# Performance work log

Hardware: AMD Instinct MI355X
Metric: run time of the kernel (lower is better)

Reference implementation:

```python
import jax, jax.numpy as jnp
import numpy as np

BN_EPS = 1e-5


def _gin_layer(x, agg, W1, b1, W2, b2, gamma, beta):
    # GINConv with eps=0: h = MLP(x + sum_{j in N(i)} x_j)
    h = x + agg
    h = jax.nn.relu(h @ W1 + b1)
    h = jax.nn.relu(h @ W2 + b2)
    # BatchNorm1d, training mode (batch statistics, biased variance)
    mean = jnp.mean(h, axis=0)
    var = jnp.var(h, axis=0)
    return (h - mean) * jax.lax.rsqrt(var + BN_EPS) * gamma + beta


def setup_inputs() -> dict:
    key = jax.random.key(0)
    ks = jax.random.split(key, 10)
    N, E, D_IN, D_H, D_OUT = 100000, 1600000, 128, 128, 128
    s = lambda fi, fo: (2.0 / (fi + fo)) ** 0.5
    return {
        "x": jax.random.normal(ks[0], (N, D_IN), dtype=jnp.float32),
        "edge_index": jax.random.randint(ks[1], (2, E), 0, N, dtype=jnp.int64),
        "W1a": jax.random.normal(ks[2], (D_IN, D_H), dtype=jnp.float32) * s(D_IN, D_H),
        "b1a": jnp.zeros((D_H,), jnp.float32),
        "W1b": jax.random.normal(ks[3], (D_H, D_H), dtype=jnp.float32) * s(D_H, D_H),
        "b1b": jnp.zeros((D_H,), jnp.float32),
        "g1": jnp.ones((D_H,), jnp.float32),
        "be1": jnp.zeros((D_H,), jnp.float32),
        "W2a": jax.random.normal(ks[4], (D_H, D_H), dtype=jnp.float32) * s(D_H, D_H),
        "b2a": jnp.zeros((D_H,), jnp.float32),
        "W2b": jax.random.normal(ks[5], (D_H, D_OUT), dtype=jnp.float32) * s(D_H, D_OUT),
        "b2b": jnp.zeros((D_OUT,), jnp.float32),
        "g2": jnp.ones((D_OUT,), jnp.float32),
        "be2": jnp.zeros((D_OUT,), jnp.float32),
    }


def reference(x, edge_index, W1a, b1a, W1b, b1b, g1, be1,
              W2a, b2a, W2b, b2b, g2, be2):
    N = x.shape[0]
    src, dst = edge_index[0], edge_index[1]
    # layer 1: scatter-add neighbor features into targets
    agg = jax.ops.segment_sum(x[src], dst, num_segments=N)
    h = _gin_layer(x, agg, W1a, b1a, W1b, b1b, g1, be1)
    # layer 2
    agg = jax.ops.segment_sum(h[src], dst, num_segments=N)
    h = _gin_layer(h, agg, W2a, b2a, W2b, b2b, g2, be2)
    return h
```

## Files before the change

kernel.cpp:

```cpp
#include <hip/hip_runtime.h>
#include <hip/hip_bf16.h>

typedef unsigned int u32;
typedef unsigned short u16;
typedef short bf16x8 __attribute__((ext_vector_type(8)));
typedef float f32x4 __attribute__((ext_vector_type(4)));

static __device__ __forceinline__ float bf_lo(u32 v) { return __uint_as_float(v << 16); }
static __device__ __forceinline__ float bf_hi(u32 v) { return __uint_as_float(v & 0xffff0000u); }
static __device__ __forceinline__ u16 f2bf(float f) {
    u32 u = __float_as_uint(f);
    u32 r = u + 0x7fffu + ((u >> 16) & 1u);
    return (u16)(r >> 16);
}
static __device__ __forceinline__ u32 pack2(float a, float b) {
    return ((u32)f2bf(b) << 16) | (u32)f2bf(a);
}

__global__ __launch_bounds__(256) void prep_k(const float* __restrict__ x,
                                              u32* __restrict__ out2, int total4,
                                              const int* __restrict__ edst,
                                              int* __restrict__ gcount, int E, int NB,
                                              const float* __restrict__ Wa,
                                              const float* __restrict__ Wb,
                                              const float* __restrict__ Wc,
                                              const float* __restrict__ Wd,
                                              u16* __restrict__ Wf)
{
    int b = blockIdx.x, t = threadIdx.x;
    if (b < 2048) {
        for (int i = b * 256 + t; i < total4; i += 2048 * 256) {
            float4 v = reinterpret_cast<const float4*>(x)[i];
            out2[2 * i + 0] = pack2(v.x, v.y);
            out2[2 * i + 1] = pack2(v.z, v.w);
        }
    } else if (b < 2304) {
        __shared__ int lh[1024];
        for (int i = t; i < 1024; i += 256) lh[i] = 0;
        __syncthreads();
        for (int e = (b - 2048) * 256 + t; e < E; e += 256 * 256)
            atomicAdd(&lh[edst[e] >> 7], 1);
        __syncthreads();
        for (int bb = t; bb < NB; bb += 256)
            if (lh[bb]) atomicAdd(&gcount[bb], lh[bb]);
    } else {
        int g = (b - 2304) * 256 + t;
        int which = g >> 14;
        int tt = g & 16383;
        const float* W = which == 0 ? Wa : which == 1 ? Wb : which == 2 ? Wc : Wd;
        int j  = tt & 7;
        int l  = (tt >> 3) & 63;
        int nb = (tt >> 9) & 7;
        int kg = (tt >> 12) & 3;
        int k  = kg * 32 + (l >> 4) * 8 + j;
        int n  = nb * 16 + (l & 15);
        Wf[g] = f2bf(W[k * 128 + n]);
    }
}

__global__ __launch_bounds__(1024) void bscan_k(const int* __restrict__ gcount,
                                                int* __restrict__ goffs,
                                                int* __restrict__ gcur, int NB)
{
    __shared__ int s[1024];
    int t = threadIdx.x;
    int v = (t < NB) ? gcount[t] : 0;
    s[t] = v; __syncthreads();
    for (int d = 1; d < 1024; d <<= 1) {
        int x = (t >= d) ? s[t - d] : 0;
        __syncthreads();
        s[t] += x;
        __syncthreads();
    }
    if (t < NB) { int o = s[t] - v; goffs[t] = o; gcur[t] = o; }
    if (t == NB - 1) goffs[NB] = s[t];
}

__global__ __launch_bounds__(256) void bfill_k(const int* __restrict__ esrc,
                                               const int* __restrict__ edst,
                                               int* __restrict__ gcur,
                                               u32* __restrict__ bpacked, int E, int NB)
{
    __shared__ int lh[1024];
    __shared__ int lbase[1024];
    int t = threadIdx.x;
    for (int i = t; i < 1024; i += 256) lh[i] = 0;
    __syncthreads();
    int per = (E + gridDim.x - 1) / gridDim.x;
    int lo = blockIdx.x * per;
    int hi = lo + per; if (hi > E) hi = E;
    for (int e = lo + t; e < hi; e += 256) atomicAdd(&lh[edst[e] >> 7], 1);
    __syncthreads();
    for (int b = t; b < NB; b += 256) {
        int c = lh[b];
        lbase[b] = c ? atomicAdd(&gcur[b], c) : 0;
    }
    __syncthreads();
    for (int i = t; i < 1024; i += 256) lh[i] = 0;
    __syncthreads();
    for (int e = lo + t; e < hi; e += 256) {
        int d = edst[e];
        int b = d >> 7;
        int idx = atomicAdd(&lh[b], 1);
        bpacked[lbase[b] + idx] = ((u32)(d & 127) << 17) | (u32)esrc[e];
    }
}

__global__ __launch_bounds__(256) void fsort_k(const u32* __restrict__ bpacked,
                                               const int* __restrict__ goffs,
                                               int* __restrict__ slots,
                                               int* __restrict__ offs,
                                               int* __restrict__ deg, int N)
{
    __shared__ int cnt[128];
    __shared__ int roff[128];
    __shared__ int sb[128];
    int b = blockIdx.x, t = threadIdx.x;
    int start = goffs[b], end = goffs[b + 1];
    if (t < 128) cnt[t] = 0;
    __syncthreads();
    for (int e = start + t; e < end; e += 256)
        atomicAdd(&cnt[bpacked[e] >> 17], 1);
    __syncthreads();
    if (t < 128) sb[t] = cnt[t];
    __syncthreads();
    for (int d = 1; d < 128; d <<= 1) {
        int x = (t < 128 && t >= d) ? sb[t - d] : 0;
        __syncthreads();
        if (t < 128) sb[t] += x;
        __syncthreads();
    }
    if (t < 128) roff[t] = sb[t] - cnt[t];
    __syncthreads();
    int row0 = b * 128;
    if (t < 128 && row0 + t < N) {
        offs[row0 + t] = start + roff[t];
        deg[row0 + t]  = cnt[t];
    }
    if (t < 128) cnt[t] = 0;
    __syncthreads();
    for (int e = start + t; e < end; e += 256) {
        u32 pk = bpacked[e];
        int local = (int)(pk >> 17);
        int idx = atomicAdd(&cnt[local], 1);
        slots[start + roff[local] + idx] = (int)(pk & 0x1FFFF);
    }
}

#define ROWP(s) reinterpret_cast<const u32*>(xbase + ((size_t)(u32)(s) << 8))

template<int MODE>
__global__ __launch_bounds__(256) void gather_k(const u32* __restrict__ xb2,
                                                const int* __restrict__ offs,
                                                const int* __restrict__ deg,
                                                const int* __restrict__ slots,
                                                const float* __restrict__ stats_in,
                                                const float* __restrict__ g_in,
                                                const float* __restrict__ be_in,
                                                u32* __restrict__ xa2, int N)
{
    __shared__ float sc[128], sh[128];
    int t = threadIdx.x;
    if (MODE == 1) {
        if (t < 128) {
            float invN = 1.0f / (float)N;
            float mean = stats_in[t] * invN;
            float var  = stats_in[128 + t] * invN - mean * mean;
            float s = g_in[t] * rsqrtf(var + 1e-5f);
            sc[t] = s;
            sh[t] = be_in[t] - mean * s;
        }
        __syncthreads();
    }

    int row = blockIdx.x * 4 + (t >> 6);
    if (row >= N) return;
    int lane = t & 63;
    const char* xbase = (const char*)xb2;

    u32 self = ROWP(row)[lane];
    float ax0 = bf_lo(self), ay0 = bf_hi(self);
    float ax1 = 0.f, ay1 = 0.f, ax2 = 0.f, ay2 = 0.f, ax3 = 0.f, ay3 = 0.f;

    int ustart = __builtin_amdgcn_readfirstlane(offs[row]);
    int udg    = __builtin_amdgcn_readfirstlane(deg[row]);

    int e = 0;
    for (; e + 16 <= udg; e += 16) {
        int s0 = slots[ustart + e + 0],  s1 = slots[ustart + e + 1];
        int s2 = slots[ustart + e + 2],  s3 = slots[ustart + e + 3];
        int s4 = slots[ustart + e + 4],  s5 = slots[ustart + e + 5];
        int s6 = slots[ustart + e + 6],  s7 = slots[ustart + e + 7];
        int s8 = slots[ustart + e + 8],  s9 = slots[ustart + e + 9];
        int sA = slots[ustart + e + 10], sB = slots[ustart + e + 11];
        int sC = slots[ustart + e + 12], sD = slots[ustart + e + 13];
        int sE = slots[ustart + e + 14], sF = slots[ustart + e + 15];
        u32 v0 = ROWP(s0)[lane], v1 = ROWP(s1)[lane];
        u32 v2 = ROWP(s2)[lane], v3 = ROWP(s3)[lane];
        u32 v4 = ROWP(s4)[lane], v5 = ROWP(s5)[lane];
        u32 v6 = ROWP(s6)[lane], v7 = ROWP(s7)[lane];
        u32 v8 = ROWP(s8)[lane], v9 = ROWP(s9)[lane];
        u32 vA = ROWP(sA)[lane], vB = ROWP(sB)[lane];
        u32 vC = ROWP(sC)[lane], vD = ROWP(sD)[lane];
        u32 vE = ROWP(sE)[lane], vF = ROWP(sF)[lane];
        ax0 += bf_lo(v0); ay0 += bf_hi(v0);  ax1 += bf_lo(v1); ay1 += bf_hi(v1);
        ax2 += bf_lo(v2); ay2 += bf_hi(v2);  ax3 += bf_lo(v3); ay3 += bf_hi(v3);
        ax0 += bf_lo(v4); ay0 += bf_hi(v4);  ax1 += bf_lo(v5); ay1 += bf_hi(v5);
        ax2 += bf_lo(v6); ay2 += bf_hi(v6);  ax3 += bf_lo(v7); ay3 += bf_hi(v7);
        ax0 += bf_lo(v8); ay0 += bf_hi(v8);  ax1 += bf_lo(v9); ay1 += bf_hi(v9);
        ax2 += bf_lo(vA); ay2 += bf_hi(vA);  ax3 += bf_lo(vB); ay3 += bf_hi(vB);
        ax0 += bf_lo(vC); ay0 += bf_hi(vC);  ax1 += bf_lo(vD); ay1 += bf_hi(vD);
        ax2 += bf_lo(vE); ay2 += bf_hi(vE);  ax3 += bf_lo(vF); ay3 += bf_hi(vF);
    }
    int k = udg - e;
    if (k) {
        int s0 = slots[ustart + e + 0],  s1 = slots[ustart + e + 1];
        int s2 = slots[ustart + e + 2],  s3 = slots[ustart + e + 3];
        int s4 = slots[ustart + e + 4],  s5 = slots[ustart + e + 5];
        int s6 = slots[ustart + e + 6],  s7 = slots[ustart + e + 7];
        int s8 = slots[ustart + e + 8],  s9 = slots[ustart + e + 9];
        int sA = slots[ustart + e + 10], sB = slots[ustart + e + 11];
        int sC = slots[ustart + e + 12], sD = slots[ustart + e + 13];
        int sE = slots[ustart + e + 14];
        u32 v0 = 0, v1 = 0, v2 = 0, v3 = 0, v4 = 0, v5 = 0, v6 = 0, v7 = 0;
        u32 v8 = 0, v9 = 0, vA = 0, vB = 0, vC = 0, vD = 0, vE = 0;
        v0 = ROWP(s0)[lane];
        if (k > 1)  v1 = ROWP(s1)[lane];
        if (k > 2)  v2 = ROWP(s2)[lane];
        if (k > 3)  v3 = ROWP(s3)[lane];
        if (k > 4)  v4 = ROWP(s4)[lane];
        if (k > 5)  v5 = ROWP(s5)[lane];
        if (k > 6)  v6 = ROWP(s6)[lane];
        if (k > 7)  v7 = ROWP(s7)[lane];
        if (k > 8)  v8 = ROWP(s8)[lane];
        if (k > 9)  v9 = ROWP(s9)[lane];
        if (k > 10) vA = ROWP(sA)[lane];
        if (k > 11) vB = ROWP(sB)[lane];
        if (k > 12) vC = ROWP(sC)[lane];
        if (k > 13) vD = ROWP(sD)[lane];
        if (k > 14) vE = ROWP(sE)[lane];
        ax0 += bf_lo(v0); ay0 += bf_hi(v0);  ax1 += bf_lo(v1); ay1 += bf_hi(v1);
        ax2 += bf_lo(v2); ay2 += bf_hi(v2);  ax3 += bf_lo(v3); ay3 += bf_hi(v3);
        ax0 += bf_lo(v4); ay0 += bf_hi(v4);  ax1 += bf_lo(v5); ay1 += bf_hi(v5);
        ax2 += bf_lo(v6); ay2 += bf_hi(v6);  ax3 += bf_lo(v7); ay3 += bf_hi(v7);
        ax0 += bf_lo(v8); ay0 += bf_hi(v8);  ax1 += bf_lo(v9); ay1 += bf_hi(v9);
        ax2 += bf_lo(vA); ay2 += bf_hi(vA);  ax3 += bf_lo(vB); ay3 += bf_hi(vB);
        ax0 += bf_lo(vC); ay0 += bf_hi(vC);  ax1 += bf_lo(vD); ay1 += bf_hi(vD);
        ax2 += bf_lo(vE); ay2 += bf_hi(vE);
    }

    float ax = (ax0 + ax1) + (ax2 + ax3);
    float ay = (ay0 + ay1) + (ay2 + ay3);
    if (MODE == 1) {
        float d1 = (float)(udg + 1);
        ax = sc[2 * lane]     * ax + d1 * sh[2 * lane];
        ay = sc[2 * lane + 1] * ay + d1 * sh[2 * lane + 1];
    }
    xa2[(size_t)row * 64 + lane] = pack2(ax, ay);
}

__global__ __launch_bounds__(256) void mlp_mfma_k(
    const u16* __restrict__ xa,
    const u16* __restrict__ wfa, const float* __restrict__ ba,
    const u16* __restrict__ wfb, const float* __restrict__ bb,
    u16* __restrict__ hb_out, float* __restrict__ partial, int N)
{
    __shared__ short ta[64 * 128];
    __shared__ float ssum[256];

    int t = threadIdx.x;
    int w = t >> 6, l = t & 63;
    int row0 = blockIdx.x * 64;

    for (int c = t; c < 1024; c += 256) {
        int r = c >> 4, ci = c & 15;
        int dst = (r * 128 + ci * 8) ^ ((r & 7) << 3);
        f32x4 v;
        if (row0 + r < N)
            v = *reinterpret_cast<const f32x4*>(xa + ((size_t)(row0 + r) * 128 + ci * 8));
        else
            v = f32x4{0.f, 0.f, 0.f, 0.f};
        *reinterpret_cast<f32x4*>(ta + dst) = v;
    }

    bf16x8 wf[2][4];
#pragma unroll
    for (int nr = 0; nr < 2; ++nr) {
        int nb = 2 * w + nr;
#pragma unroll
        for (int kg = 0; kg < 4; ++kg)
            wf[nr][kg] = *reinterpret_cast<const bf16x8*>(
                wfa + ((size_t)((kg * 8 + nb) * 64 + l)) * 8);
    }
    __syncthreads();

    int rr = l & 15;
    int kg8 = l >> 4;

    f32x4 acc[4][2];
#pragma unroll
    for (int mr = 0; mr < 4; ++mr)
#pragma unroll
        for (int nr = 0; nr < 2; ++nr)
            acc[mr][nr] = f32x4{0.f, 0.f, 0.f, 0.f};

#pragma unroll
    for (int mr = 0; mr < 4; ++mr) {
        int r = mr * 16 + rr;
        bf16x8 af[4];
#pragma unroll
        for (int kg = 0; kg < 4; ++kg) {
            int idx = (r * 128 + kg * 32 + kg8 * 8) ^ ((r & 7) << 3);
            af[kg] = *reinterpret_cast<const bf16x8*>(ta + idx);
        }
#pragma unroll
        for (int nr = 0; nr < 2; ++nr)
#pragma unroll
            for (int kg = 0; kg < 4; ++kg)
                acc[mr][nr] = __builtin_amdgcn_mfma_f32_16x16x32_bf16(
                    af[kg], wf[nr][kg], acc[mr][nr], 0, 0, 0);
    }
    __syncthreads();

    bf16x8 wf2[2][4];
#pragma unroll
    for (int nr = 0; nr < 2; ++nr) {
        int nb = 2 * w + nr;
#pragma unroll
        for (int kg = 0; kg < 4; ++kg)
            wf2[nr][kg] = *reinterpret_cast<const bf16x8*>(
                wfb + ((size_t)((kg * 8 + nb) * 64 + l)) * 8);
    }

    int colb = w * 32;
    float b0 = ba[colb + rr];
    float b1 = ba[colb + 16 + rr];
#pragma unroll
    for (int mr = 0; mr < 4; ++mr)
#pragma unroll
        for (int nr = 0; nr < 2; ++nr) {
            float bb_ = nr ? b1 : b0;
            int col = colb + nr * 16 + rr;
#pragma unroll
            for (int reg = 0; reg < 4; ++reg) {
                int row = mr * 16 + kg8 * 4 + reg;
                float v = fmaxf(acc[mr][nr][reg] + bb_, 0.0f);
                ta[(row * 128 + col) ^ ((row & 7) << 3)] = (short)f2bf(v);
            }
        }
    __syncthreads();

#pragma unroll
    for (int mr = 0; mr < 4; ++mr)
#pragma unroll
        for (int nr = 0; nr < 2; ++nr)
            acc[mr][nr] = f32x4{0.f, 0.f, 0.f, 0.f};

#pragma unroll
    for (int mr = 0; mr < 4; ++mr) {
        int r = mr * 16 + rr;
        bf16x8 af[4];
#pragma unroll
        for (int kg = 0; kg < 4; ++kg) {
            int idx = (r * 128 + kg * 32 + kg8 * 8) ^ ((r & 7) << 3);
            af[kg] = *reinterpret_cast<const bf16x8*>(ta + idx);
        }
#pragma unroll
        for (int nr = 0; nr < 2; ++nr)
#pragma unroll
            for (int kg = 0; kg < 4; ++kg)
                acc[mr][nr] = __builtin_amdgcn_mfma_f32_16x16x32_bf16(
                    af[kg], wf2[nr][kg], acc[mr][nr], 0, 0, 0);
    }

    float c0 = bb[colb + rr];
    float c1 = bb[colb + 16 + rr];
    float s0 = 0.f, q0 = 0.f, s1 = 0.f, q1 = 0.f;
#pragma unroll
    for (int mr = 0; mr < 4; ++mr) {
#pragma unroll
        for (int reg = 0; reg < 4; ++reg) {
            int row = row0 + mr * 16 + kg8 * 4 + reg;
            bool ok = row < N;
            float v0 = fmaxf(acc[mr][0][reg] + c0, 0.0f);
            float v1 = fmaxf(acc[mr][1][reg] + c1, 0.0f);
            if (ok) {
                hb_out[(size_t)row * 128 + colb + rr]      = f2bf(v0);
                hb_out[(size_t)row * 128 + colb + 16 + rr] = f2bf(v1);
                s0 += v0; q0 += v0 * v0;
                s1 += v1; q1 += v1 * v1;
            }
        }
    }
    s0 += __shfl_xor(s0, 16); s0 += __shfl_xor(s0, 32);
    q0 += __shfl_xor(q0, 16); q0 += __shfl_xor(q0, 32);
    s1 += __shfl_xor(s1, 16); s1 += __shfl_xor(s1, 32);
    q1 += __shfl_xor(q1, 16); q1 += __shfl_xor(q1, 32);
    if (kg8 == 0) {
        ssum[colb + rr]            = s0;
        ssum[128 + colb + rr]      = q0;
        ssum[colb + 16 + rr]       = s1;
        ssum[128 + colb + 16 + rr] = q1;
    }
    __syncthreads();
    partial[(size_t)blockIdx.x * 256 + t] = ssum[t];
}

__global__ __launch_bounds__(256) void reduce_k(const float* __restrict__ partial,
                                                float* __restrict__ stats, int nrows)
{
    int t = threadIdx.x;
    int chunk = (nrows + gridDim.x - 1) / gridDim.x;
    int lo = blockIdx.x * chunk;
    int hi = lo + chunk; if (hi > nrows) hi = nrows;
    float acc = 0.f;
    for (int r = lo; r < hi; ++r)
        acc += partial[(size_t)r * 256 + t];
    if (hi > lo) atomicAdd(&stats[t], acc);
}

__global__ __launch_bounds__(256) void bn_apply_bf_k(
    const u32* __restrict__ h2b, const float* __restrict__ stats,
    const float* __restrict__ gamma, const float* __restrict__ beta,
    float* __restrict__ out, int N)
{
    __shared__ float sc[128], sh[128];
    int t = threadIdx.x;
    if (t < 128) {
        float invN = 1.0f / (float)N;
        float mean = stats[t] * invN;
        float var  = stats[128 + t] * invN - mean * mean;
        float s = gamma[t] * rsqrtf(var + 1e-5f);
        sc[t] = s;
        sh[t] = beta[t] - mean * s;
    }
    __syncthreads();
    int total2 = N * 64;
    for (int i = blockIdx.x * 256 + t; i < total2; i += gridDim.x * 256) {
        u32 v = h2b[i];
        int c = (i & 63) * 2;
        float2 o;
        o.x = bf_lo(v) * sc[c]     + sh[c];
        o.y = bf_hi(v) * sc[c + 1] + sh[c + 1];
        reinterpret_cast<float2*>(out)[i] = o;
    }
}

extern "C" void kernel_launch(void* const* d_in, const int* in_sizes, int n_in,
                              void* d_out, int out_size, void* d_ws, size_t ws_size,
                              hipStream_t stream)
{
    const float* x   = (const float*)d_in[0];
    const int*   ei  = (const int*)d_in[1];
    const float* W1a = (const float*)d_in[2];
    const float* b1a = (const float*)d_in[3];
    const float* W1b = (const float*)d_in[4];
    const float* b1b = (const float*)d_in[5];
    const float* g1  = (const float*)d_in[6];
    const float* be1 = (const float*)d_in[7];
    const float* W2a = (const float*)d_in[8];
    const float* b2a = (const float*)d_in[9];
    const float* W2b = (const float*)d_in[10];
    const float* b2b = (const float*)d_in[11];
    const float* g2  = (const float*)d_in[12];
    const float* be2 = (const float*)d_in[13];

    const int N = in_sizes[0] / 128;
    const int E = in_sizes[1] / 2;
    const int* esrc = ei;
    const int* edst = ei + E;
    const int NB = (N + 127) >> 7;

    const int mblocks = (N + 63) / 64;
    const int gblocks = (N + 3) / 4;

    char* p = (char*)d_ws;
    const size_t featb = (size_t)N * 128 * sizeof(u16);
    u16* xa = (u16*)p;            p += featb;
    u16* h1 = (u16*)p;            p += featb;
    u16* xb = (u16*)p;            p += featb;
    u16* wf = (u16*)p;            p += 4 * 16384 * sizeof(u16);
    int* slots = (int*)p;         p += (size_t)E * sizeof(int) + 64;
    int* deg   = (int*)p;         p += (size_t)N * sizeof(int);
    int* offs  = (int*)p;         p += (size_t)N * sizeof(int);
    int* gcount = (int*)p;        p += 1024 * sizeof(int);
    int* goffs  = (int*)p;        p += 1032 * sizeof(int);
    int* gcur   = (int*)p;        p += 1024 * sizeof(int);
    float* stats = (float*)p;     p += 512 * sizeof(float);
    float* partial = (float*)p;   p += (size_t)mblocks * 256 * sizeof(float);
    u32* bpacked = (u32*)xa;

    u16* wf1a = wf;
    u16* wf1b = wf + 16384;
    u16* wf2a = wf + 32768;
    u16* wf2b = wf + 49152;
    float* stats1 = stats;
    float* stats2 = stats + 256;

    float* h = (float*)d_out;

    hipMemsetAsync(gcount, 0, 1024 * sizeof(int), stream);
    prep_k<<<2560, 256, 0, stream>>>(x, (u32*)xb, N * 32,
                                     edst, gcount, E, NB,
                                     W1a, W1b, W2a, W2b, wf);
    bscan_k<<<1, 1024, 0, stream>>>(gcount, goffs, gcur, NB);
    bfill_k<<<256, 256, 0, stream>>>(esrc, edst, gcur, bpacked, E, NB);
    fsort_k<<<NB, 256, 0, stream>>>(bpacked, goffs, slots, offs, deg, N);
    hipMemsetAsync(stats, 0, 512 * sizeof(float), stream);

    gather_k<0><<<gblocks, 256, 0, stream>>>((const u32*)xb, offs, deg, slots,
                                             nullptr, nullptr, nullptr, (u32*)xa, N);
    mlp_mfma_k<<<mblocks, 256, 0, stream>>>(xa, wf1a, b1a, wf1b, b1b,
                                            h1, partial, N);
    reduce_k<<<32, 256, 0, stream>>>(partial, stats1, mblocks);

    gather_k<1><<<gblocks, 256, 0, stream>>>((const u32*)h1, offs, deg, slots,
                                             stats1, g1, be1, (u32*)xa, N);
    mlp_mfma_k<<<mblocks, 256, 0, stream>>>(xa, wf2a, b2a, wf2b, b2b,
                                            h1, partial, N);
    reduce_k<<<32, 256, 0, stream>>>(partial, stats2, mblocks);

    bn_apply_bf_k<<<2048, 256, 0, stream>>>((const u32*)h1, stats2, g2, be2, h, N);
}
```

Measured before the change: 275.4 us.

## Pad CSR neighbor lists to multiples of 16 with zero-row sentinels

The CSR build now pads each row's neighbor list to a multiple of 16 entries, filling the extras with indices of zero rows appended after the feature buffers. This takes an extra count pass, a second scan and a split sort kernel. In exchange the gather loop has no predicated tail: it unrolls by 32 with one 16-wide remainder, aiming to remove divergent tail loads and give more loads in flight. The cost is extra slot memory, redundant zero-row loads (about 7.5 per row on average at degree 16), and two more kernel launches.

```diff
diff --git a/kernel.cpp b/kernel.cpp
--- a/kernel.cpp
+++ b/kernel.cpp
@@ -58,13 +58,13 @@
     }
 }
 
-__global__ __launch_bounds__(1024) void bscan_k(const int* __restrict__ gcount,
-                                                int* __restrict__ goffs,
-                                                int* __restrict__ gcur, int NB)
+__global__ __launch_bounds__(1024) void bscan_k(const int* __restrict__ cnt,
+                                                int* __restrict__ outoffs,
+                                                int* __restrict__ outcur, int n)
 {
     __shared__ int s[1024];
     int t = threadIdx.x;
-    int v = (t < NB) ? gcount[t] : 0;
+    int v = (t < n) ? cnt[t] : 0;
     s[t] = v; __syncthreads();
     for (int d = 1; d < 1024; d <<= 1) {
         int x = (t >= d) ? s[t - d] : 0;
@@ -72,8 +72,8 @@
         s[t] += x;
         __syncthreads();
     }
-    if (t < NB) { int o = s[t] - v; goffs[t] = o; gcur[t] = o; }
-    if (t == NB - 1) goffs[NB] = s[t];
+    if (t < n) { int o = s[t] - v; outoffs[t] = o; if (outcur) outcur[t] = o; }
+    if (t == n - 1) outoffs[n] = s[t];
 }
 
 __global__ __launch_bounds__(256) void bfill_k(const int* __restrict__ esrc,
@@ -106,23 +106,47 @@
     }
 }
 
-__global__ __launch_bounds__(256) void fsort_k(const u32* __restrict__ bpacked,
-                                               const int* __restrict__ goffs,
-                                               int* __restrict__ slots,
-                                               int* __restrict__ offs,
-                                               int* __restrict__ deg, int N)
+__global__ __launch_bounds__(256) void fsortA_k(const u32* __restrict__ bpacked,
+                                                const int* __restrict__ goffs,
+                                                int* __restrict__ deg,
+                                                int* __restrict__ pbtotal, int N)
+{
+    __shared__ int cnt[128];
+    __shared__ int red[256];
+    int b = blockIdx.x, t = threadIdx.x;
+    int start = goffs[b], end = goffs[b + 1];
+    if (t < 128) cnt[t] = 0;
+    __syncthreads();
+    for (int e = start + t; e < end; e += 256)
+        atomicAdd(&cnt[bpacked[e] >> 17], 1);
+    __syncthreads();
+    int row0 = b * 128;
+    if (t < 128 && row0 + t < N) deg[row0 + t] = cnt[t];
+    red[t] = (t < 128) ? ((cnt[t] + 15) & ~15) : 0;
+    __syncthreads();
+    for (int d = 128; d >= 1; d >>= 1) {
+        if (t < d) red[t] += red[t + d];
+        __syncthreads();
+    }
+    if (t == 0) pbtotal[b] = red[0];
+}
+
+__global__ __launch_bounds__(256) void fsortB_k(const u32* __restrict__ bpacked,
+                                                const int* __restrict__ goffs,
+                                                const int* __restrict__ pbase,
+                                                const int* __restrict__ deg,
+                                                int* __restrict__ slots,
+                                                int* __restrict__ offs, int N)
 {
     __shared__ int cnt[128];
     __shared__ int roff[128];
     __shared__ int sb[128];
     int b = blockIdx.x, t = threadIdx.x;
     int start = goffs[b], end = goffs[b + 1];
-    if (t < 128) cnt[t] = 0;
-    __syncthreads();
-    for (int e = start + t; e < end; e += 256)
-        atomicAdd(&cnt[bpacked[e] >> 17], 1);
-    __syncthreads();
-    if (t < 128) sb[t] = cnt[t];
+    int row0 = b * 128;
+    int myc = (t < 128 && row0 + t < N) ? deg[row0 + t] : 0;
+    int pd = (myc + 15) & ~15;
+    if (t < 128) { sb[t] = pd; cnt[t] = 0; }
     __syncthreads();
     for (int d = 1; d < 128; d <<= 1) {
         int x = (t < 128 && t >= d) ? sb[t - d] : 0;
@@ -130,20 +154,22 @@
         if (t < 128) sb[t] += x;
         __syncthreads();
     }
-    if (t < 128) roff[t] = sb[t] - cnt[t];
-    __syncthreads();
-    int row0 = b * 128;
-    if (t < 128 && row0 + t < N) {
-        offs[row0 + t] = start + roff[t];
-        deg[row0 + t]  = cnt[t];
-    }
-    if (t < 128) cnt[t] = 0;
+    int base = pbase[b];
+    if (t < 128) {
+        roff[t] = sb[t] - pd;
+        if (row0 + t < N) offs[row0 + t] = base + roff[t];
+    }
     __syncthreads();
     for (int e = start + t; e < end; e += 256) {
         u32 pk = bpacked[e];
         int local = (int)(pk >> 17);
         int idx = atomicAdd(&cnt[local], 1);
-        slots[start + roff[local] + idx] = (int)(pk & 0x1FFFF);
+        slots[base + roff[local] + idx] = (int)(pk & 0x1FFFF);
+    }
+    __syncthreads();
+    if (t < 128) {
+        int o = base + roff[t];
+        for (int i = myc; i < pd; ++i) slots[o + i] = N + (i & 15);
     }
 }
 
@@ -184,9 +210,60 @@
 
     int ustart = __builtin_amdgcn_readfirstlane(offs[row]);
     int udg    = __builtin_amdgcn_readfirstlane(deg[row]);
+    int pdg    = (udg + 15) & ~15;
 
     int e = 0;
-    for (; e + 16 <= udg; e += 16) {
+    for (; e + 32 <= pdg; e += 32) {
+        int s0 = slots[ustart + e + 0],  s1 = slots[ustart + e + 1];
+        int s2 = slots[ustart + e + 2],  s3 = slots[ustart + e + 3];
+        int s4 = slots[ustart + e + 4],  s5 = slots[ustart + e + 5];
+        int s6 = slots[ustart + e + 6],  s7 = slots[ustart + e + 7];
+        int s8 = slots[ustart + e + 8],  s9 = slots[ustart + e + 9];
+        int sA = slots[ustart + e + 10], sB = slots[ustart + e + 11];
+        int sC = slots[ustart + e + 12], sD = slots[ustart + e + 13];
+        int sE = slots[ustart + e + 14], sF = slots[ustart + e + 15];
+        int sG = slots[ustart + e + 16], sH = slots[ustart + e + 17];
+        int sI = slots[ustart + e + 18], sJ = slots[ustart + e + 19];
+        int sK = slots[ustart + e + 20], sL = slots[ustart + e + 21];
+        int sM = slots[ustart + e + 22], sN_ = slots[ustart + e + 23];
+        int sO = slots[ustart + e + 24], sP = slots[ustart + e + 25];
+        int sQ = slots[ustart + e + 26], sR = slots[ustart + e + 27];
+        int sS = slots[ustart + e + 28], sT = slots[ustart + e + 29];
+        int sU = slots[ustart + e + 30], sV = slots[ustart + e + 31];
+        u32 v0 = ROWP(s0)[lane], v1 = ROWP(s1)[lane];
+        u32 v2 = ROWP(s2)[lane], v3 = ROWP(s3)[lane];
+        u32 v4 = ROWP(s4)[lane], v5 = ROWP(s5)[lane];
+        u32 v6 = ROWP(s6)[lane], v7 = ROWP(s7)[lane];
+        u32 v8 = ROWP(s8)[lane], v9 = ROWP(s9)[lane];
+        u32 vA = ROWP(sA)[lane], vB = ROWP(sB)[lane];
+        u32 vC = ROWP(sC)[lane], vD = ROWP(sD)[lane];
+        u32 vE = ROWP(sE)[lane], vF = ROWP(sF)[lane];
+        u32 vG = ROWP(sG)[lane], vH = ROWP(sH)[lane];
+        u32 vI = ROWP(sI)[lane], vJ = ROWP(sJ)[lane];
+        u32 vK = ROWP(sK)[lane], vL = ROWP(sL)[lane];
+        u32 vM = ROWP(sM)[lane], vN = ROWP(sN_)[lane];
+        u32 vO = ROWP(sO)[lane], vP = ROWP(sP)[lane];
+        u32 vQ = ROWP(sQ)[lane], vR = ROWP(sR)[lane];
+        u32 vS = ROWP(sS)[lane], vT = ROWP(sT)[lane];
+        u32 vU = ROWP(sU)[lane], vV = ROWP(sV)[lane];
+        ax0 += bf_lo(v0); ay0 += bf_hi(v0);  ax1 += bf_lo(v1); ay1 += bf_hi(v1);
+        ax2 += bf_lo(v2); ay2 += bf_hi(v2);  ax3 += bf_lo(v3); ay3 += bf_hi(v3);
+        ax0 += bf_lo(v4); ay0 += bf_hi(v4);  ax1 += bf_lo(v5); ay1 += bf_hi(v5);
+        ax2 += bf_lo(v6); ay2 += bf_hi(v6);  ax3 += bf_lo(v7); ay3 += bf_hi(v7);
+        ax0 += bf_lo(v8); ay0 += bf_hi(v8);  ax1 += bf_lo(v9); ay1 += bf_hi(v9);
+        ax2 += bf_lo(vA); ay2 += bf_hi(vA);  ax3 += bf_lo(vB); ay3 += bf_hi(vB);
+        ax0 += bf_lo(vC); ay0 += bf_hi(vC);  ax1 += bf_lo(vD); ay1 += bf_hi(vD);
+        ax2 += bf_lo(vE); ay2 += bf_hi(vE);  ax3 += bf_lo(vF); ay3 += bf_hi(vF);
+        ax0 += bf_lo(vG); ay0 += bf_hi(vG);  ax1 += bf_lo(vH); ay1 += bf_hi(vH);
+        ax2 += bf_lo(vI); ay2 += bf_hi(vI);  ax3 += bf_lo(vJ); ay3 += bf_hi(vJ);
+        ax0 += bf_lo(vK); ay0 += bf_hi(vK);  ax1 += bf_lo(vL); ay1 += bf_hi(vL);
+        ax2 += bf_lo(vM); ay2 += bf_hi(vM);  ax3 += bf_lo(vN); ay3 += bf_hi(vN);
+        ax0 += bf_lo(vO); ay0 += bf_hi(vO);  ax1 += bf_lo(vP); ay1 += bf_hi(vP);
+        ax2 += bf_lo(vQ); ay2 += bf_hi(vQ);  ax3 += bf_lo(vR); ay3 += bf_hi(vR);
+        ax0 += bf_lo(vS); ay0 += bf_hi(vS);  ax1 += bf_lo(vT); ay1 += bf_hi(vT);
+        ax2 += bf_lo(vU); ay2 += bf_hi(vU);  ax3 += bf_lo(vV); ay3 += bf_hi(vV);
+    }
+    if (e < pdg) {
         int s0 = slots[ustart + e + 0],  s1 = slots[ustart + e + 1];
         int s2 = slots[ustart + e + 2],  s3 = slots[ustart + e + 3];
         int s4 = slots[ustart + e + 4],  s5 = slots[ustart + e + 5];
@@ -212,42 +289,6 @@
         ax0 += bf_lo(vC); ay0 += bf_hi(vC);  ax1 += bf_lo(vD); ay1 += bf_hi(vD);
         ax2 += bf_lo(vE); ay2 += bf_hi(vE);  ax3 += bf_lo(vF); ay3 += bf_hi(vF);
     }
-    int k = udg - e;
-    if (k) {
-        int s0 = slots[ustart + e + 0],  s1 = slots[ustart + e + 1];
-        int s2 = slots[ustart + e + 2],  s3 = slots[ustart + e + 3];
-        int s4 = slots[ustart + e + 4],  s5 = slots[ustart + e + 5];
-        int s6 = slots[ustart + e + 6],  s7 = slots[ustart + e + 7];
-        int s8 = slots[ustart + e + 8],  s9 = slots[ustart + e + 9];
-        int sA = slots[ustart + e + 10], sB = slots[ustart + e + 11];
-        int sC = slots[ustart + e + 12], sD = slots[ustart + e + 13];
-        int sE = slots[ustart + e + 14];
-        u32 v0 = 0, v1 = 0, v2 = 0, v3 = 0, v4 = 0, v5 = 0, v6 = 0, v7 = 0;
-        u32 v8 = 0, v9 = 0, vA = 0, vB = 0, vC = 0, vD = 0, vE = 0;
-        v0 = ROWP(s0)[lane];
-        if (k > 1)  v1 = ROWP(s1)[lane];
-        if (k > 2)  v2 = ROWP(s2)[lane];
-        if (k > 3)  v3 = ROWP(s3)[lane];
-        if (k > 4)  v4 = ROWP(s4)[lane];
-        if (k > 5)  v5 = ROWP(s5)[lane];
-        if (k > 6)  v6 = ROWP(s6)[lane];
-        if (k > 7)  v7 = ROWP(s7)[lane];
-        if (k > 8)  v8 = ROWP(s8)[lane];
-        if (k > 9)  v9 = ROWP(s9)[lane];
-        if (k > 10) vA = ROWP(sA)[lane];
-        if (k > 11) vB = ROWP(sB)[lane];
-        if (k > 12) vC = ROWP(sC)[lane];
-        if (k > 13) vD = ROWP(sD)[lane];
-        if (k > 14) vE = ROWP(sE)[lane];
-        ax0 += bf_lo(v0); ay0 += bf_hi(v0);  ax1 += bf_lo(v1); ay1 += bf_hi(v1);
-        ax2 += bf_lo(v2); ay2 += bf_hi(v2);  ax3 += bf_lo(v3); ay3 += bf_hi(v3);
-        ax0 += bf_lo(v4); ay0 += bf_hi(v4);  ax1 += bf_lo(v5); ay1 += bf_hi(v5);
-        ax2 += bf_lo(v6); ay2 += bf_hi(v6);  ax3 += bf_lo(v7); ay3 += bf_hi(v7);
-        ax0 += bf_lo(v8); ay0 += bf_hi(v8);  ax1 += bf_lo(v9); ay1 += bf_hi(v9);
-        ax2 += bf_lo(vA); ay2 += bf_hi(vA);  ax3 += bf_lo(vB); ay3 += bf_hi(vB);
-        ax0 += bf_lo(vC); ay0 += bf_hi(vC);  ax1 += bf_lo(vD); ay1 += bf_hi(vD);
-        ax2 += bf_lo(vE); ay2 += bf_hi(vE);
-    }
 
     float ax = (ax0 + ax1) + (ax2 + ax3);
     float ay = (ay0 + ay1) + (ay2 + ay3);
@@ -475,17 +516,20 @@
     const int gblocks = (N + 3) / 4;
 
     char* p = (char*)d_ws;
-    const size_t featb = (size_t)N * 128 * sizeof(u16);
+    const size_t featb  = (size_t)N * 128 * sizeof(u16);
+    const size_t featbz = (size_t)(N + 16) * 128 * sizeof(u16);
     u16* xa = (u16*)p;            p += featb;
-    u16* h1 = (u16*)p;            p += featb;
-    u16* xb = (u16*)p;            p += featb;
+    u16* h1 = (u16*)p;            p += featbz;
+    u16* xb = (u16*)p;            p += featbz;
     u16* wf = (u16*)p;            p += 4 * 16384 * sizeof(u16);
-    int* slots = (int*)p;         p += (size_t)E * sizeof(int) + 64;
+    int* slots = (int*)p;         p += ((size_t)E + 15 * (size_t)N) * sizeof(int) + 64;
     int* deg   = (int*)p;         p += (size_t)N * sizeof(int);
     int* offs  = (int*)p;         p += (size_t)N * sizeof(int);
     int* gcount = (int*)p;        p += 1024 * sizeof(int);
     int* goffs  = (int*)p;        p += 1032 * sizeof(int);
     int* gcur   = (int*)p;        p += 1024 * sizeof(int);
+    int* pbtotal = (int*)p;       p += 1024 * sizeof(int);
+    int* pbase   = (int*)p;       p += 1032 * sizeof(int);
     float* stats = (float*)p;     p += 512 * sizeof(float);
     float* partial = (float*)p;   p += (size_t)mblocks * 256 * sizeof(float);
     u32* bpacked = (u32*)xa;
@@ -500,12 +544,16 @@
     float* h = (float*)d_out;
 
     hipMemsetAsync(gcount, 0, 1024 * sizeof(int), stream);
+    hipMemsetAsync(xb + (size_t)N * 128, 0, 16 * 256, stream);
+    hipMemsetAsync(h1 + (size_t)N * 128, 0, 16 * 256, stream);
     prep_k<<<2560, 256, 0, stream>>>(x, (u32*)xb, N * 32,
                                      edst, gcount, E, NB,
                                      W1a, W1b, W2a, W2b, wf);
     bscan_k<<<1, 1024, 0, stream>>>(gcount, goffs, gcur, NB);
     bfill_k<<<256, 256, 0, stream>>>(esrc, edst, gcur, bpacked, E, NB);
-    fsort_k<<<NB, 256, 0, stream>>>(bpacked, goffs, slots, offs, deg, N);
+    fsortA_k<<<NB, 256, 0, stream>>>(bpacked, goffs, deg, pbtotal, N);
+    bscan_k<<<1, 1024, 0, stream>>>(pbtotal, pbase, (int*)nullptr, NB);
+    fsortB_k<<<NB, 256, 0, stream>>>(bpacked, goffs, pbase, deg, slots, offs, N);
     hipMemsetAsync(stats, 0, 512 * sizeof(float), stream);
 
     gather_k<0><<<gblocks, 256, 0, stream>>>((const u32*)xb, offs, deg, slots,
```

Result: slower. 287.2 us (+4.3%).
